# Performance work log

Measured on AMD Instinct MI355X. Metric: run time of the kernel, lower is better.

Reference implementation:

```python
import jax, jax.numpy as jnp
import numpy as np

C = 8        # in_channels (forced: C//8 must be 1 for the broadcast matmul to work)
CQ = C // 8  # query/key channels = 1


def setup_inputs() -> dict:
    key = jax.random.key(0)
    ks = jax.random.split(key, 7)
    B, H, W = 16, 512, 512
    x = jax.random.normal(ks[0], (B, C, H, W), dtype=jnp.float32)
    # 1x1 conv weights stored as [out_ch, in_ch]
    sq = 1.0 / np.sqrt(C)
    Wq = jax.random.uniform(ks[1], (CQ, C), jnp.float32, -sq, sq)
    bq = jax.random.uniform(ks[2], (CQ,), jnp.float32, -sq, sq)
    Wk = jax.random.uniform(ks[3], (CQ, C), jnp.float32, -sq, sq)
    bk = jax.random.uniform(ks[4], (CQ,), jnp.float32, -sq, sq)
    Wv = jax.random.uniform(ks[5], (C, C), jnp.float32, -sq, sq)
    bv = jax.random.uniform(ks[6], (C,), jnp.float32, -sq, sq)
    return {"x": x, "Wq": Wq, "bq": bq, "Wk": Wk, "bk": bk, "Wv": Wv, "bv": bv}


def reference(x, Wq, bq, Wk, bk, Wv, bv):
    # 1x1 convs == per-pixel channel mixing
    q = jnp.einsum('bchw,oc->bohw', x, Wq) + bq[None, :, None, None]   # [B,1,H,W]
    k = jnp.einsum('bchw,oc->bohw', x, Wk) + bk[None, :, None, None]   # [B,1,H,W]
    v = jnp.einsum('bchw,oc->bohw', x, Wv) + bv[None, :, None, None]   # [B,C,H,W]
    # attention over rows: attn[b,o,i,j] = sum_w q[b,o,i,w] * k[b,o,j,w]  (no scaling, as in source)
    attn = jnp.einsum('boiw,bojw->boij', q, k)                          # [B,1,H,H]
    attn = jax.nn.softmax(attn, axis=-1)
    # broadcast matmul: [B,1,H,H] @ [B,C,H,W] -> [B,C,H,W]
    out = jnp.einsum('boij,bcjw->bciw', attn, v)
    return out
```

## Files before the change

### kernel.cpp

```cpp
#include <hip/hip_runtime.h>

constexpr int B = 16, C = 8, H = 512, W = 512;
constexpr int HW = H * W;

typedef short bf16x8 __attribute__((ext_vector_type(8)));
typedef float f32x4 __attribute__((ext_vector_type(4)));

__device__ __forceinline__ unsigned short f2bf(float f) {
    union { float f; unsigned u; } v; v.f = f;
    unsigned r = (v.u + 0x7FFFu + ((v.u >> 16) & 1u)) >> 16;
    return (unsigned short)r;
}

__global__ __launch_bounds__(256) void qkv_kernel(
    const float* __restrict__ x, const float* __restrict__ Wq, const float* __restrict__ bq,
    const float* __restrict__ Wk, const float* __restrict__ bk, const float* __restrict__ Wv,
    float* __restrict__ q, float* __restrict__ k, unsigned short* __restrict__ v)
{
    int t = blockIdx.x * 256 + threadIdx.x;
    int b = t / (HW / 4);
    int p = (t % (HW / 4)) * 4;
    const float* xb = x + (size_t)b * C * HW + p;
    float4 aq = make_float4(bq[0], bq[0], bq[0], bq[0]);
    float4 ak = make_float4(bk[0], bk[0], bk[0], bk[0]);
    float vacc[8][4] = {};
#pragma unroll
    for (int cc = 0; cc < 8; ++cc) {
        float4 xv = *reinterpret_cast<const float4*>(xb + (size_t)cc * HW);
        float wq = Wq[cc], wk = Wk[cc];
        aq.x = fmaf(wq, xv.x, aq.x); aq.y = fmaf(wq, xv.y, aq.y);
        aq.z = fmaf(wq, xv.z, aq.z); aq.w = fmaf(wq, xv.w, aq.w);
        ak.x = fmaf(wk, xv.x, ak.x); ak.y = fmaf(wk, xv.y, ak.y);
        ak.z = fmaf(wk, xv.z, ak.z); ak.w = fmaf(wk, xv.w, ak.w);
#pragma unroll
        for (int c = 0; c < 8; ++c) {
            float wv = Wv[c * 8 + cc];
            vacc[c][0] = fmaf(wv, xv.x, vacc[c][0]);
            vacc[c][1] = fmaf(wv, xv.y, vacc[c][1]);
            vacc[c][2] = fmaf(wv, xv.z, vacc[c][2]);
            vacc[c][3] = fmaf(wv, xv.w, vacc[c][3]);
        }
    }
    *reinterpret_cast<float4*>(q + (size_t)b * HW + p) = aq;
    *reinterpret_cast<float4*>(k + (size_t)b * HW + p) = ak;
#pragma unroll
    for (int c = 0; c < 8; ++c) {
        ushort4 pk;
        pk.x = f2bf(vacc[c][0]); pk.y = f2bf(vacc[c][1]);
        pk.z = f2bf(vacc[c][2]); pk.w = f2bf(vacc[c][3]);
        *reinterpret_cast<ushort4*>(v + ((size_t)(b * 8 + c)) * HW + p) = pk;
    }
}

__global__ __launch_bounds__(256) void transpose_kernel(
    const unsigned short* __restrict__ v, unsigned short* __restrict__ vt)
{
    __shared__ int lds[64][65];
    int bc = blockIdx.y;
    int j0 = (blockIdx.x >> 3) * 64;
    int w0 = (blockIdx.x & 7) * 64;
    const unsigned short* vp = v + (size_t)bc * HW;
    unsigned short* vtp = vt + (size_t)bc * HW;
    int t = threadIdx.x;
    int jr = t >> 4, c4 = (t & 15) * 4;
#pragma unroll
    for (int rr = 0; rr < 4; ++rr) {
        int j = jr + rr * 16;
        ushort4 d = *reinterpret_cast<const ushort4*>(vp + (size_t)(j0 + j) * W + w0 + c4);
        lds[j][c4 + 0] = d.x; lds[j][c4 + 1] = d.y;
        lds[j][c4 + 2] = d.z; lds[j][c4 + 3] = d.w;
    }
    __syncthreads();
#pragma unroll
    for (int rr = 0; rr < 4; ++rr) {
        int w = jr + rr * 16;
        ushort4 d;
        d.x = (unsigned short)lds[c4 + 0][w];
        d.y = (unsigned short)lds[c4 + 1][w];
        d.z = (unsigned short)lds[c4 + 2][w];
        d.w = (unsigned short)lds[c4 + 3][w];
        *reinterpret_cast<ushort4*>(vtp + (size_t)(w0 + w) * H + j0 + c4) = d;
    }
}

__global__ __launch_bounds__(256) void qk_gemm_kernel(
    const float* __restrict__ q, const float* __restrict__ k, float* __restrict__ attn)
{
    __shared__ float As[16][132];
    __shared__ float Bs[16][132];
    int b  = blockIdx.z;
    int i0 = blockIdx.y * 128;
    int j0 = blockIdx.x * 128;
    const float* Qb = q + (size_t)b * HW;
    const float* Kb = k + (size_t)b * HW;
    int t  = threadIdx.x;
    int tx = t % 16, ty = t / 16;
    int sc = t % 16, sr0 = t / 16;
    float acc[8][8] = {};
    for (int w0 = 0; w0 < W; w0 += 16) {
        __syncthreads();
#pragma unroll
        for (int p = 0; p < 8; ++p) {
            int r = sr0 + 16 * p;
            As[sc][r] = Qb[(size_t)(i0 + r) * W + w0 + sc];
            Bs[sc][r] = Kb[(size_t)(j0 + r) * W + w0 + sc];
        }
        __syncthreads();
#pragma unroll
        for (int kk = 0; kk < 16; ++kk) {
            float a[8], bb[8];
            *reinterpret_cast<float4*>(&a[0])  = *reinterpret_cast<const float4*>(&As[kk][ty * 8]);
            *reinterpret_cast<float4*>(&a[4])  = *reinterpret_cast<const float4*>(&As[kk][ty * 8 + 4]);
            *reinterpret_cast<float4*>(&bb[0]) = *reinterpret_cast<const float4*>(&Bs[kk][tx * 8]);
            *reinterpret_cast<float4*>(&bb[4]) = *reinterpret_cast<const float4*>(&Bs[kk][tx * 8 + 4]);
#pragma unroll
            for (int m = 0; m < 8; ++m)
#pragma unroll
                for (int n = 0; n < 8; ++n)
                    acc[m][n] = fmaf(a[m], bb[n], acc[m][n]);
        }
    }
    float* Cb = attn + (size_t)b * H * H;
#pragma unroll
    for (int m = 0; m < 8; ++m) {
        int row = i0 + ty * 8 + m;
        *reinterpret_cast<float4*>(&Cb[(size_t)row * H + j0 + tx * 8]) =
            make_float4(acc[m][0], acc[m][1], acc[m][2], acc[m][3]);
        *reinterpret_cast<float4*>(&Cb[(size_t)row * H + j0 + tx * 8 + 4]) =
            make_float4(acc[m][4], acc[m][5], acc[m][6], acc[m][7]);
    }
}

__global__ __launch_bounds__(256) void softmax_kernel(
    const float* __restrict__ attn, unsigned short* __restrict__ attn_bf)
{
    int gid  = blockIdx.x * 256 + threadIdx.x;
    int row  = gid >> 6;
    int lane = gid & 63;
    const float* rp = attn + (size_t)row * H;
    float4 v0 = *reinterpret_cast<const float4*>(&rp[lane * 8]);
    float4 v1 = *reinterpret_cast<const float4*>(&rp[lane * 8 + 4]);
    float m = fmaxf(fmaxf(fmaxf(v0.x, v0.y), fmaxf(v0.z, v0.w)),
                    fmaxf(fmaxf(v1.x, v1.y), fmaxf(v1.z, v1.w)));
#pragma unroll
    for (int off = 32; off > 0; off >>= 1) m = fmaxf(m, __shfl_xor(m, off, 64));
    v0.x = __expf(v0.x - m); v0.y = __expf(v0.y - m);
    v0.z = __expf(v0.z - m); v0.w = __expf(v0.w - m);
    v1.x = __expf(v1.x - m); v1.y = __expf(v1.y - m);
    v1.z = __expf(v1.z - m); v1.w = __expf(v1.w - m);
    float s = v0.x + v0.y + v0.z + v0.w + v1.x + v1.y + v1.z + v1.w;
#pragma unroll
    for (int off = 32; off > 0; off >>= 1) s += __shfl_xor(s, off, 64);
    float inv = 1.0f / s;
    unsigned short* bp = attn_bf + (size_t)row * H + lane * 8;
    ushort4 o0, o1;
    o0.x = f2bf(v0.x * inv); o0.y = f2bf(v0.y * inv);
    o0.z = f2bf(v0.z * inv); o0.w = f2bf(v0.w * inv);
    o1.x = f2bf(v1.x * inv); o1.y = f2bf(v1.y * inv);
    o1.z = f2bf(v1.z * inv); o1.w = f2bf(v1.w * inv);
    *reinterpret_cast<ushort4*>(bp)     = o0;
    *reinterpret_cast<ushort4*>(bp + 4) = o1;
}

__global__ __launch_bounds__(256, 2) void pv_mfma_kernel(
    const unsigned short* __restrict__ attn_bf,
    const unsigned short* __restrict__ vt,
    const float* __restrict__ bv, float* __restrict__ out)
{
    __shared__ char Ash[2][128 * 128];
    __shared__ char Bsh[2][128 * 128];

    int b  = blockIdx.z;
    int i0 = blockIdx.y * 128;
    int n0 = blockIdx.x * 128;
    int tid  = threadIdx.x;
    int lane = tid & 63, wv = tid >> 6;
    int wm = wv >> 1, wn = wv & 1;

    const char* Abase = (const char*)(attn_bf + (size_t)b * H * H);
    const char* Bbase = (const char*)(vt + (size_t)b * C * HW + (size_t)n0 * H);

    int rsub = lane >> 3;
    int slot = lane & 7;
    int swsl = (slot ^ rsub) << 4;

    f32x4 acc[4][4] = {};

#define STAGE(buf, kt)                                                                   \
    {                                                                                    \
        int koff = (kt) * 128;                                                           \
        _Pragma("unroll")                                                                \
        for (int qq = 0; qq < 4; ++qq) {                                                 \
            int chunk = wv * 4 + qq;                                                     \
            int r = chunk * 8 + rsub;                                                    \
            __builtin_amdgcn_global_load_lds(                                            \
                (const __attribute__((address_space(1))) unsigned int*)                  \
                    (Abase + (size_t)(i0 + r) * 1024 + koff + swsl),                     \
                (__attribute__((address_space(3))) unsigned int*)(Ash[buf] + chunk * 1024), \
                16, 0, 0);                                                               \
            __builtin_amdgcn_global_load_lds(                                            \
                (const __attribute__((address_space(1))) unsigned int*)                  \
                    (Bbase + (size_t)r * 1024 + koff + swsl),                            \
                (__attribute__((address_space(3))) unsigned int*)(Bsh[buf] + chunk * 1024), \
                16, 0, 0);                                                               \
        }                                                                                \
    }

    STAGE(0, 0);
    int cur = 0;
    for (int kt = 0; kt < 8; ++kt) {
        __syncthreads();
        if (kt + 1 < 8) STAGE(cur ^ 1, kt + 1);

        const char* Ab = Ash[cur];
        const char* Bb = Bsh[cur];
        bf16x8 af[4][2], bf[4][2];
#pragma unroll
        for (int m = 0; m < 4; ++m) {
            int row = wm * 64 + m * 16 + (lane & 15);
            int base = row * 128 + ((lane >> 4) << 4);
            int sw = (row & 7) << 4;
            af[m][0] = *reinterpret_cast<const bf16x8*>(Ab + ((base)      ^ sw));
            af[m][1] = *reinterpret_cast<const bf16x8*>(Ab + ((base + 64) ^ sw));
        }
#pragma unroll
        for (int n = 0; n < 4; ++n) {
            int row = wn * 64 + n * 16 + (lane & 15);
            int base = row * 128 + ((lane >> 4) << 4);
            int sw = (row & 7) << 4;
            bf[n][0] = *reinterpret_cast<const bf16x8*>(Bb + ((base)      ^ sw));
            bf[n][1] = *reinterpret_cast<const bf16x8*>(Bb + ((base + 64) ^ sw));
        }
#pragma unroll
        for (int ks = 0; ks < 2; ++ks)
#pragma unroll
            for (int m = 0; m < 4; ++m)
#pragma unroll
                for (int n = 0; n < 4; ++n)
                    acc[m][n] = __builtin_amdgcn_mfma_f32_16x16x32_bf16(
                        af[m][ks], bf[n][ks], acc[m][n], 0, 0, 0);
        cur ^= 1;
    }
#undef STAGE

    int cc = n0 >> 9;
    int w0 = n0 & 511;
    float bias = bv[cc];
    float* outb = out + ((size_t)(b * C + cc)) * HW;
#pragma unroll
    for (int m = 0; m < 4; ++m) {
        int i = i0 + wm * 64 + m * 16 + ((lane >> 4) << 2);
#pragma unroll
        for (int n = 0; n < 4; ++n) {
            int w = w0 + wn * 64 + n * 16 + (lane & 15);
#pragma unroll
            for (int r = 0; r < 4; ++r)
                outb[(size_t)(i + r) * W + w] = acc[m][n][r] + bias;
        }
    }
}

extern "C" void kernel_launch(void* const* d_in, const int* in_sizes, int n_in,
                              void* d_out, int out_size, void* d_ws, size_t ws_size,
                              hipStream_t stream) {
    const float* x  = (const float*)d_in[0];
    const float* Wq = (const float*)d_in[1];
    const float* bq = (const float*)d_in[2];
    const float* Wk = (const float*)d_in[3];
    const float* bk = (const float*)d_in[4];
    const float* Wv = (const float*)d_in[5];
    const float* bv = (const float*)d_in[6];
    float* out = (float*)d_out;

    float* q = (float*)d_ws;
    float* k = q + (size_t)B * HW;
    float* attnf = k + (size_t)B * HW;
    unsigned short* attnb = (unsigned short*)(attnf + (size_t)B * H * H);
    unsigned short* vtb = attnb + (size_t)B * H * H;
    unsigned short* v = (unsigned short*)d_out;

    qkv_kernel<<<B * HW / 4 / 256, 256, 0, stream>>>(x, Wq, bq, Wk, bk, Wv, q, k, v);
    transpose_kernel<<<dim3(64, B * C), 256, 0, stream>>>(v, vtb);
    qk_gemm_kernel<<<dim3(H / 128, H / 128, B), 256, 0, stream>>>(q, k, attnf);
    softmax_kernel<<<(B * H * 64) / 256, 256, 0, stream>>>(attnf, attnb);
    pv_mfma_kernel<<<dim3(32, 4, B), 256, 0, stream>>>(attnb, vtb, bv, out);
}
```

Baseline: 378.3 us.

## Fuse QKV projection with V transpose and use split-bf16 MFMA for QK

```diff
diff --git a/kernel.cpp b/kernel.cpp
--- a/kernel.cpp
+++ b/kernel.cpp
@@ -11,123 +11,189 @@
     unsigned r = (v.u + 0x7FFFu + ((v.u >> 16) & 1u)) >> 16;
     return (unsigned short)r;
 }
-
-__global__ __launch_bounds__(256) void qkv_kernel(
+__device__ __forceinline__ float bf2f(unsigned short u) {
+    union { unsigned u; float f; } v; v.u = (unsigned)u << 16;
+    return v.f;
+}
+__device__ __forceinline__ void split1(float a, unsigned short& h, unsigned short& l) {
+    h = f2bf(a);
+    l = f2bf(a - bf2f(h));
+}
+
+__global__ __launch_bounds__(256) void qkv_fused_kernel(
     const float* __restrict__ x, const float* __restrict__ Wq, const float* __restrict__ bq,
     const float* __restrict__ Wk, const float* __restrict__ bk, const float* __restrict__ Wv,
-    float* __restrict__ q, float* __restrict__ k, unsigned short* __restrict__ v)
+    unsigned short* __restrict__ qh, unsigned short* __restrict__ ql,
+    unsigned short* __restrict__ kh, unsigned short* __restrict__ kl,
+    unsigned short* __restrict__ vt)
 {
-    int t = blockIdx.x * 256 + threadIdx.x;
-    int b = t / (HW / 4);
-    int p = (t % (HW / 4)) * 4;
-    const float* xb = x + (size_t)b * C * HW + p;
-    float4 aq = make_float4(bq[0], bq[0], bq[0], bq[0]);
-    float4 ak = make_float4(bk[0], bk[0], bk[0], bk[0]);
-    float vacc[8][4] = {};
-#pragma unroll
-    for (int cc = 0; cc < 8; ++cc) {
-        float4 xv = *reinterpret_cast<const float4*>(xb + (size_t)cc * HW);
-        float wq = Wq[cc], wk = Wk[cc];
-        aq.x = fmaf(wq, xv.x, aq.x); aq.y = fmaf(wq, xv.y, aq.y);
-        aq.z = fmaf(wq, xv.z, aq.z); aq.w = fmaf(wq, xv.w, aq.w);
-        ak.x = fmaf(wk, xv.x, ak.x); ak.y = fmaf(wk, xv.y, ak.y);
-        ak.z = fmaf(wk, xv.z, ak.z); ak.w = fmaf(wk, xv.w, ak.w);
-#pragma unroll
-        for (int c = 0; c < 8; ++c) {
-            float wv = Wv[c * 8 + cc];
-            vacc[c][0] = fmaf(wv, xv.x, vacc[c][0]);
-            vacc[c][1] = fmaf(wv, xv.y, vacc[c][1]);
-            vacc[c][2] = fmaf(wv, xv.z, vacc[c][2]);
-            vacc[c][3] = fmaf(wv, xv.w, vacc[c][3]);
-        }
-    }
-    *reinterpret_cast<float4*>(q + (size_t)b * HW + p) = aq;
-    *reinterpret_cast<float4*>(k + (size_t)b * HW + p) = ak;
-#pragma unroll
-    for (int c = 0; c < 8; ++c) {
-        ushort4 pk;
-        pk.x = f2bf(vacc[c][0]); pk.y = f2bf(vacc[c][1]);
-        pk.z = f2bf(vacc[c][2]); pk.w = f2bf(vacc[c][3]);
-        *reinterpret_cast<ushort4*>(v + ((size_t)(b * 8 + c)) * HW + p) = pk;
-    }
-}
-
-__global__ __launch_bounds__(256) void transpose_kernel(
-    const unsigned short* __restrict__ v, unsigned short* __restrict__ vt)
-{
-    __shared__ int lds[64][65];
-    int bc = blockIdx.y;
+    __shared__ int ldsv[4][64][65];
+    int b  = blockIdx.y;
     int j0 = (blockIdx.x >> 3) * 64;
     int w0 = (blockIdx.x & 7) * 64;
-    const unsigned short* vp = v + (size_t)bc * HW;
-    unsigned short* vtp = vt + (size_t)bc * HW;
-    int t = threadIdx.x;
+    const float* xb = x + (size_t)b * C * HW;
+    int t  = threadIdx.x;
     int jr = t >> 4, c4 = (t & 15) * 4;
+
+    float wq[8], wk[8], wv[8][8];
+#pragma unroll
+    for (int cc = 0; cc < 8; ++cc) {
+        wq[cc] = Wq[cc]; wk[cc] = Wk[cc];
+#pragma unroll
+        for (int c = 0; c < 8; ++c) wv[c][cc] = Wv[c * 8 + cc];
+    }
+    float bq0 = bq[0], bk0 = bk[0];
+
 #pragma unroll
     for (int rr = 0; rr < 4; ++rr) {
         int j = jr + rr * 16;
-        ushort4 d = *reinterpret_cast<const ushort4*>(vp + (size_t)(j0 + j) * W + w0 + c4);
-        lds[j][c4 + 0] = d.x; lds[j][c4 + 1] = d.y;
-        lds[j][c4 + 2] = d.z; lds[j][c4 + 3] = d.w;
+        size_t prow = (size_t)(j0 + j) * W + w0 + c4;
+        float4 aq = make_float4(bq0, bq0, bq0, bq0);
+        float4 ak = make_float4(bk0, bk0, bk0, bk0);
+        float vacc[8][4] = {};
+#pragma unroll
+        for (int cc = 0; cc < 8; ++cc) {
+            float4 xv = *reinterpret_cast<const float4*>(xb + (size_t)cc * HW + prow);
+            aq.x = fmaf(wq[cc], xv.x, aq.x); aq.y = fmaf(wq[cc], xv.y, aq.y);
+            aq.z = fmaf(wq[cc], xv.z, aq.z); aq.w = fmaf(wq[cc], xv.w, aq.w);
+            ak.x = fmaf(wk[cc], xv.x, ak.x); ak.y = fmaf(wk[cc], xv.y, ak.y);
+            ak.z = fmaf(wk[cc], xv.z, ak.z); ak.w = fmaf(wk[cc], xv.w, ak.w);
+#pragma unroll
+            for (int c = 0; c < 8; ++c) {
+                vacc[c][0] = fmaf(wv[c][cc], xv.x, vacc[c][0]);
+                vacc[c][1] = fmaf(wv[c][cc], xv.y, vacc[c][1]);
+                vacc[c][2] = fmaf(wv[c][cc], xv.z, vacc[c][2]);
+                vacc[c][3] = fmaf(wv[c][cc], xv.w, vacc[c][3]);
+            }
+        }
+        size_t qoff = (size_t)b * HW + prow;
+        ushort4 h4, l4;
+        split1(aq.x, h4.x, l4.x); split1(aq.y, h4.y, l4.y);
+        split1(aq.z, h4.z, l4.z); split1(aq.w, h4.w, l4.w);
+        *reinterpret_cast<ushort4*>(qh + qoff) = h4;
+        *reinterpret_cast<ushort4*>(ql + qoff) = l4;
+        split1(ak.x, h4.x, l4.x); split1(ak.y, h4.y, l4.y);
+        split1(ak.z, h4.z, l4.z); split1(ak.w, h4.w, l4.w);
+        *reinterpret_cast<ushort4*>(kh + qoff) = h4;
+        *reinterpret_cast<ushort4*>(kl + qoff) = l4;
+#pragma unroll
+        for (int cp = 0; cp < 4; ++cp)
+#pragma unroll
+            for (int i = 0; i < 4; ++i)
+                ldsv[cp][j][c4 + i] =
+                    (unsigned)f2bf(vacc[2 * cp][i]) | ((unsigned)f2bf(vacc[2 * cp + 1][i]) << 16);
     }
     __syncthreads();
 #pragma unroll
-    for (int rr = 0; rr < 4; ++rr) {
-        int w = jr + rr * 16;
-        ushort4 d;
-        d.x = (unsigned short)lds[c4 + 0][w];
-        d.y = (unsigned short)lds[c4 + 1][w];
-        d.z = (unsigned short)lds[c4 + 2][w];
-        d.w = (unsigned short)lds[c4 + 3][w];
-        *reinterpret_cast<ushort4*>(vtp + (size_t)(w0 + w) * H + j0 + c4) = d;
-    }
-}
-
-__global__ __launch_bounds__(256) void qk_gemm_kernel(
-    const float* __restrict__ q, const float* __restrict__ k, float* __restrict__ attn)
+    for (int cp = 0; cp < 4; ++cp) {
+#pragma unroll
+        for (int rr = 0; rr < 4; ++rr) {
+            int w = jr + rr * 16;
+            int d0 = ldsv[cp][c4 + 0][w];
+            int d1 = ldsv[cp][c4 + 1][w];
+            int d2 = ldsv[cp][c4 + 2][w];
+            int d3 = ldsv[cp][c4 + 3][w];
+            ushort4 e, o;
+            e.x = (unsigned short)d0; o.x = (unsigned short)(d0 >> 16);
+            e.y = (unsigned short)d1; o.y = (unsigned short)(d1 >> 16);
+            e.z = (unsigned short)d2; o.z = (unsigned short)(d2 >> 16);
+            e.w = (unsigned short)d3; o.w = (unsigned short)(d3 >> 16);
+            size_t voff = (size_t)(w0 + w) * H + j0 + c4;
+            *reinterpret_cast<ushort4*>(vt + ((size_t)(b * 8 + 2 * cp))     * HW + voff) = e;
+            *reinterpret_cast<ushort4*>(vt + ((size_t)(b * 8 + 2 * cp + 1)) * HW + voff) = o;
+        }
+    }
+}
+
+__global__ __launch_bounds__(256, 2) void qk_mfma_kernel(
+    const unsigned short* __restrict__ qh_, const unsigned short* __restrict__ ql_,
+    const unsigned short* __restrict__ kh_, const unsigned short* __restrict__ kl_,
+    float* __restrict__ attn)
 {
-    __shared__ float As[16][132];
-    __shared__ float Bs[16][132];
+    __shared__ char Ash[2][16384];
+    __shared__ char Bsh[2][16384];
     int b  = blockIdx.z;
     int i0 = blockIdx.y * 128;
     int j0 = blockIdx.x * 128;
-    const float* Qb = q + (size_t)b * HW;
-    const float* Kb = k + (size_t)b * HW;
-    int t  = threadIdx.x;
-    int tx = t % 16, ty = t / 16;
-    int sc = t % 16, sr0 = t / 16;
-    float acc[8][8] = {};
-    for (int w0 = 0; w0 < W; w0 += 16) {
+    int tid  = threadIdx.x;
+    int lane = tid & 63, wv4 = tid >> 6;
+    int wm = wv4 >> 1, wn = wv4 & 1;
+
+    const char* qhB = (const char*)qh_ + (size_t)b * HW * 2;
+    const char* qlB = (const char*)ql_ + (size_t)b * HW * 2;
+    const char* khB = (const char*)kh_ + (size_t)b * HW * 2;
+    const char* klB = (const char*)kl_ + (size_t)b * HW * 2;
+
+    int ls  = (lane & 7) ^ (lane >> 3);
+    int hsel = ls & 1, ssel = ls >> 1;
+
+    f32x4 acc[4][4] = {};
+
+#define STAGE(buf, kt)                                                                    \
+    {                                                                                     \
+        _Pragma("unroll")                                                                 \
+        for (int pass = 0; pass < 4; ++pass) {                                            \
+            int row = pass * 32 + wv4 * 8 + (lane >> 3);                                  \
+            const char* sA = (hsel ? qlB : qhB) + (size_t)(i0 + row) * 1024 + (kt) * 64 + ssel * 16; \
+            const char* sB = (hsel ? klB : khB) + (size_t)(j0 + row) * 1024 + (kt) * 64 + ssel * 16; \
+            __builtin_amdgcn_global_load_lds(                                             \
+                (const __attribute__((address_space(1))) unsigned int*)sA,                \
+                (__attribute__((address_space(3))) unsigned int*)(Ash[buf] + pass * 4096 + wv4 * 1024), \
+                16, 0, 0);                                                                \
+            __builtin_amdgcn_global_load_lds(                                             \
+                (const __attribute__((address_space(1))) unsigned int*)sB,                \
+                (__attribute__((address_space(3))) unsigned int*)(Bsh[buf] + pass * 4096 + wv4 * 1024), \
+                16, 0, 0);                                                                \
+        }                                                                                 \
+    }
+
+    STAGE(0, 0);
+    int cur = 0;
+    for (int kt = 0; kt < 16; ++kt) {
         __syncthreads();
-#pragma unroll
-        for (int p = 0; p < 8; ++p) {
-            int r = sr0 + 16 * p;
-            As[sc][r] = Qb[(size_t)(i0 + r) * W + w0 + sc];
-            Bs[sc][r] = Kb[(size_t)(j0 + r) * W + w0 + sc];
-        }
-        __syncthreads();
-#pragma unroll
-        for (int kk = 0; kk < 16; ++kk) {
-            float a[8], bb[8];
-            *reinterpret_cast<float4*>(&a[0])  = *reinterpret_cast<const float4*>(&As[kk][ty * 8]);
-            *reinterpret_cast<float4*>(&a[4])  = *reinterpret_cast<const float4*>(&As[kk][ty * 8 + 4]);
-            *reinterpret_cast<float4*>(&bb[0]) = *reinterpret_cast<const float4*>(&Bs[kk][tx * 8]);
-            *reinterpret_cast<float4*>(&bb[4]) = *reinterpret_cast<const float4*>(&Bs[kk][tx * 8 + 4]);
-#pragma unroll
-            for (int m = 0; m < 8; ++m)
-#pragma unroll
-                for (int n = 0; n < 8; ++n)
-                    acc[m][n] = fmaf(a[m], bb[n], acc[m][n]);
-        }
-    }
+        if (kt + 1 < 16) STAGE(cur ^ 1, kt + 1);
+
+        const char* Ab = Ash[cur];
+        const char* Bb = Bsh[cur];
+        bf16x8 ah[4], al[4], bh[4], bl[4];
+        int sr = lane >> 4;
+#pragma unroll
+        for (int m = 0; m < 4; ++m) {
+            int row = wm * 64 + m * 16 + (lane & 15);
+            int sw = row & 7;
+            ah[m] = *reinterpret_cast<const bf16x8*>(Ab + row * 128 + ((2 * sr)     ^ sw) * 16);
+            al[m] = *reinterpret_cast<const bf16x8*>(Ab + row * 128 + ((2 * sr + 1) ^ sw) * 16);
+        }
+#pragma unroll
+        for (int n = 0; n < 4; ++n) {
+            int row = wn * 64 + n * 16 + (lane & 15);
+            int sw = row & 7;
+            bh[n] = *reinterpret_cast<const bf16x8*>(Bb + row * 128 + ((2 * sr)     ^ sw) * 16);
+            bl[n] = *reinterpret_cast<const bf16x8*>(Bb + row * 128 + ((2 * sr + 1) ^ sw) * 16);
+        }
+#pragma unroll
+        for (int m = 0; m < 4; ++m)
+#pragma unroll
+            for (int n = 0; n < 4; ++n) {
+                acc[m][n] = __builtin_amdgcn_mfma_f32_16x16x32_bf16(ah[m], bh[n], acc[m][n], 0, 0, 0);
+                acc[m][n] = __builtin_amdgcn_mfma_f32_16x16x32_bf16(ah[m], bl[n], acc[m][n], 0, 0, 0);
+                acc[m][n] = __builtin_amdgcn_mfma_f32_16x16x32_bf16(al[m], bh[n], acc[m][n], 0, 0, 0);
+            }
+        cur ^= 1;
+    }
+#undef STAGE
+
     float* Cb = attn + (size_t)b * H * H;
 #pragma unroll
-    for (int m = 0; m < 8; ++m) {
-        int row = i0 + ty * 8 + m;
-        *reinterpret_cast<float4*>(&Cb[(size_t)row * H + j0 + tx * 8]) =
-            make_float4(acc[m][0], acc[m][1], acc[m][2], acc[m][3]);
-        *reinterpret_cast<float4*>(&Cb[(size_t)row * H + j0 + tx * 8 + 4]) =
-            make_float4(acc[m][4], acc[m][5], acc[m][6], acc[m][7]);
+    for (int m = 0; m < 4; ++m) {
+        int i = i0 + wm * 64 + m * 16 + ((lane >> 4) << 2);
+#pragma unroll
+        for (int n = 0; n < 4; ++n) {
+            int j = j0 + wn * 64 + n * 16 + (lane & 15);
+#pragma unroll
+            for (int r = 0; r < 4; ++r)
+                Cb[(size_t)(i + r) * H + j] = acc[m][n][r];
+        }
     }
 }
 
@@ -272,16 +338,16 @@
     const float* bv = (const float*)d_in[6];
     float* out = (float*)d_out;
 
-    float* q = (float*)d_ws;
-    float* k = q + (size_t)B * HW;
-    float* attnf = k + (size_t)B * HW;
+    unsigned short* qh = (unsigned short*)d_ws;
+    unsigned short* ql = qh + (size_t)B * HW;
+    unsigned short* kh = ql + (size_t)B * HW;
+    unsigned short* kl = kh + (size_t)B * HW;
+    float* attnf = (float*)(kl + (size_t)B * HW);
     unsigned short* attnb = (unsigned short*)(attnf + (size_t)B * H * H);
     unsigned short* vtb = attnb + (size_t)B * H * H;
-    unsigned short* v = (unsigned short*)d_out;
-
-    qkv_kernel<<<B * HW / 4 / 256, 256, 0, stream>>>(x, Wq, bq, Wk, bk, Wv, q, k, v);
-    transpose_kernel<<<dim3(64, B * C), 256, 0, stream>>>(v, vtb);
-    qk_gemm_kernel<<<dim3(H / 128, H / 128, B), 256, 0, stream>>>(q, k, attnf);
+
+    qkv_fused_kernel<<<dim3(64, B), 256, 0, stream>>>(x, Wq, bq, Wk, bk, Wv, qh, ql, kh, kl, vtb);
+    qk_mfma_kernel<<<dim3(4, 4, B), 256, 0, stream>>>(qh, ql, kh, kl, attnf);
     softmax_kernel<<<(B * H * 64) / 256, 256, 0, stream>>>(attnf, attnb);
     pv_mfma_kernel<<<dim3(32, 4, B), 256, 0, stream>>>(attnb, vtb, bv, out);
 }
```

New measurement: 325.3 us. -14.0%, faster.
